# Kernel tuning notes

Measured on AMD Instinct MI355X. Metric: run time of the kernel, lower is better.

Reference implementation:

```python
import jax, jax.numpy as jnp
import numpy as np

D_MODEL = 1024
NUM_HEADS = 16
HEAD_DIM = D_MODEL // NUM_HEADS
CLAMP = 1e9


def setup_inputs() -> dict:
    key = jax.random.key(0)
    ks = jax.random.split(key, 5)
    B, S = 2, 2048
    x = jax.random.normal(ks[0], (B, S, D_MODEL), dtype=jnp.float32)
    # causal mask, broadcastable over [B, H, S, S]
    mask = jnp.tril(jnp.ones((S, S), dtype=bool))
    Wqkv = jax.random.normal(ks[1], (D_MODEL, 3 * D_MODEL), dtype=jnp.float32) * (1.0 / np.sqrt(D_MODEL))
    bqkv = jax.random.normal(ks[2], (3 * D_MODEL,), dtype=jnp.float32) * 0.02
    Wo = jax.random.normal(ks[3], (D_MODEL, D_MODEL), dtype=jnp.float32) * (1.0 / np.sqrt(D_MODEL))
    bo = jax.random.normal(ks[4], (D_MODEL,), dtype=jnp.float32) * 0.02
    return {"x": x, "mask": mask, "Wqkv": Wqkv, "bqkv": bqkv, "Wo": Wo, "bo": bo}


def reference(x, mask, Wqkv, bqkv, Wo, bo):
    B, S, _ = x.shape
    qkv = x @ Wqkv + bqkv                               # [B, S, 3*d_model]
    qkv = qkv.reshape(B, S, NUM_HEADS, 3 * HEAD_DIM).transpose(0, 2, 1, 3)  # [B, H, S, 3*hd]
    q, k, v = jnp.split(qkv, 3, axis=-1)                # each [B, H, S, hd]
    scale = 1.0 / np.sqrt(HEAD_DIM)
    scores = jnp.einsum('bhqd,bhkd->bhqk', q, k) * scale  # [B, H, S, S]
    scores = jnp.where(mask, scores, -jnp.inf)
    scores = jnp.clip(scores, -CLAMP, CLAMP)
    attn = jax.nn.softmax(scores, axis=-1)
    values = jnp.einsum('bhqk,bhkd->bhqd', attn, v)     # [B, H, S, hd]
    values = values.transpose(0, 2, 1, 3).reshape(B, S, D_MODEL)
    return values @ Wo + bo
```

## Files before the change

kernel.cpp:

```cpp
#include <hip/hip_runtime.h>
#include <hip/hip_bf16.h>

#define S_LEN 2048
#define NHEAD 16
#define HDIM  64
#define DMODEL 1024

typedef unsigned short u16;
typedef __attribute__((ext_vector_type(8))) short short8;
typedef __attribute__((ext_vector_type(4))) float floatx4;
typedef __attribute__((ext_vector_type(4))) u16 u16x4;

__device__ __forceinline__ u16 f2bf(float f) {
  unsigned u = __builtin_bit_cast(unsigned, f);
  u += 0x7fffu + ((u >> 16) & 1u);
  return (u16)(u >> 16);
}
__device__ __forceinline__ float bf2f(u16 b) {
  unsigned u = ((unsigned)b) << 16;
  return __builtin_bit_cast(float, u);
}
__device__ __forceinline__ void gload_lds16(const void* g, void* l) {
  __builtin_amdgcn_global_load_lds((const __attribute__((address_space(1))) unsigned int*)g,
                                   (__attribute__((address_space(3))) unsigned int*)l,
                                   16, 0, 0);
}
__device__ __forceinline__ int swz(int b) { return b ^ (((b >> 7) & 7) << 4); }

#define MFMA16(a, b, c) __builtin_amdgcn_mfma_f32_16x16x32_bf16(a, b, c, 0, 0, 0)

__global__ __launch_bounds__(256) void k_prep(const float* __restrict__ x,
                                              const float* __restrict__ Wqkv,
                                              const float* __restrict__ Wo,
                                              u16* __restrict__ xh,
                                              u16* __restrict__ wh,
                                              u16* __restrict__ woh) {
  int bid = blockIdx.x, tid = threadIdx.x;
  if (bid < 4096) {
    int i = (bid * 256 + tid) * 4;
    float4 v = *(const float4*)(x + i);
    u16x4 hv = {f2bf(v.x), f2bf(v.y), f2bf(v.z), f2bf(v.w)};
    *(u16x4*)(xh + i) = hv;
    return;
  }
  __shared__ float t[32][33];
  const float* in; u16* oh; int C, bx, by;
  if (bid < 7168) { int b = bid - 4096; in = Wqkv; oh = wh;  C = 3072; bx = b % 96; by = b / 96; }
  else            { int b = bid - 7168; in = Wo;   oh = woh; C = 1024; bx = b & 31; by = b >> 5; }
  const int R = 1024;
  int c0 = bx * 32, r0 = by * 32;
  int tx = tid & 31, ty = tid >> 5;
#pragma unroll
  for (int rr = ty; rr < 32; rr += 8) t[rr][tx] = in[(size_t)(r0 + rr) * C + c0 + tx];
  __syncthreads();
#pragma unroll
  for (int rr = ty; rr < 32; rr += 8)
    oh[(size_t)(c0 + rr) * R + r0 + tx] = f2bf(t[tx][rr]);
}

__device__ __forceinline__ void gemm_main(const u16* __restrict__ A, const u16* __restrict__ B,
                                          int m0, int n0, floatx4 (&acc)[4][4],
                                          u16* sA, u16* sB) {
  const int tid = threadIdx.x, lane = tid & 63;
  const int wid = tid >> 6, wr = wid >> 1, wc = wid & 1;
  const int cl = lane & 15, hi = lane >> 4;
  const int rmask = ((cl >> 1) & 7) << 4;
  const int aoff = (wr * 4096 + cl * 64 + hi * 16) ^ rmask;
  const int boff = (wc * 4096 + cl * 64 + hi * 16) ^ rmask;
#pragma unroll
  for (int i = 0; i < 4; ++i)
#pragma unroll
    for (int j = 0; j < 4; ++j) acc[i][j] = (floatx4){0.f, 0.f, 0.f, 0.f};

  auto stage = [&](int buf, int kt) {
    int k0 = kt * 32;
#pragma unroll
    for (int it = 0; it < 2; ++it) {
      int p = (it * 256 + tid) * 16;
      int q = swz(p);
      int row = q >> 6, colb = q & 63;
      int base = buf * 8192 + (it * 256 + (tid & ~63)) * 16;
      gload_lds16((const char*)A + (size_t)(m0 + row) * 2048 + k0 * 2 + colb, (char*)sA + base);
      gload_lds16((const char*)B + (size_t)(n0 + row) * 2048 + k0 * 2 + colb, (char*)sB + base);
    }
  };
  stage(0, 0);
  __syncthreads();
  for (int kt = 0; kt < 32; ++kt) {
    int cur = kt & 1;
    if (kt + 1 < 32) stage(cur ^ 1, kt + 1);
    short8 a[4], b[4];
#pragma unroll
    for (int i = 0; i < 4; ++i) {
      a[i] = *(const short8*)((const char*)sA + cur * 8192 + aoff + i * 1024);
      b[i] = *(const short8*)((const char*)sB + cur * 8192 + boff + i * 1024);
    }
    __builtin_amdgcn_s_setprio(1);
#pragma unroll
    for (int i = 0; i < 4; ++i)
#pragma unroll
      for (int j = 0; j < 4; ++j)
        acc[i][j] = MFMA16(a[i], b[j], acc[i][j]);
    __builtin_amdgcn_s_setprio(0);
    __syncthreads();
  }
}

__device__ __forceinline__ void gemm_main_n64(const u16* __restrict__ A, const u16* __restrict__ B,
                                              int m0, int n0, floatx4 (&acc)[4][2]) {
  __shared__ __align__(16) u16 sA[2][128 * 32];
  __shared__ __align__(16) u16 sB[2][64 * 32];
  const int tid = threadIdx.x, lane = tid & 63;
  const int wid = tid >> 6, wr = wid >> 1, wc = wid & 1;
  const int cl = lane & 15, hi = lane >> 4;
  const int rmask = ((cl >> 1) & 7) << 4;
  const int aoff = (wr * 4096 + cl * 64 + hi * 16) ^ rmask;
  const int boff = (wc * 2048 + cl * 64 + hi * 16) ^ rmask;
#pragma unroll
  for (int i = 0; i < 4; ++i)
#pragma unroll
    for (int j = 0; j < 2; ++j) acc[i][j] = (floatx4){0.f, 0.f, 0.f, 0.f};

  auto stage = [&](int buf, int kt) {
    int k0 = kt * 32;
#pragma unroll
    for (int it = 0; it < 2; ++it) {
      int p = (it * 256 + tid) * 16;
      int q = swz(p);
      int row = q >> 6, colb = q & 63;
      int base = (it * 256 + (tid & ~63)) * 16;
      gload_lds16((const char*)A + (size_t)(m0 + row) * 2048 + k0 * 2 + colb, (char*)sA[buf] + base);
    }
    {
      int p = tid * 16;
      int q = swz(p);
      int row = q >> 6, colb = q & 63;
      int base = (tid & ~63) * 16;
      gload_lds16((const char*)B + (size_t)(n0 + row) * 2048 + k0 * 2 + colb, (char*)sB[buf] + base);
    }
  };
  stage(0, 0);
  __syncthreads();
  for (int kt = 0; kt < 32; ++kt) {
    int cur = kt & 1;
    if (kt + 1 < 32) stage(cur ^ 1, kt + 1);
    short8 a[4], b[2];
#pragma unroll
    for (int i = 0; i < 4; ++i)
      a[i] = *(const short8*)((const char*)sA[cur] + aoff + i * 1024);
#pragma unroll
    for (int j = 0; j < 2; ++j)
      b[j] = *(const short8*)((const char*)sB[cur] + boff + j * 1024);
    __builtin_amdgcn_s_setprio(1);
#pragma unroll
    for (int i = 0; i < 4; ++i)
#pragma unroll
      for (int j = 0; j < 2; ++j)
        acc[i][j] = MFMA16(a[i], b[j], acc[i][j]);
    __builtin_amdgcn_s_setprio(0);
    __syncthreads();
  }
}

__global__ __launch_bounds__(256) void k_qkv_gemm(const u16* __restrict__ xh,
                                                  const u16* __restrict__ wh,
                                                  const float* __restrict__ bqkv,
                                                  u16* __restrict__ Qb, u16* __restrict__ Kb,
                                                  u16* __restrict__ Vt) {
  int bid = blockIdx.y * 24 + blockIdx.x;
  int sid = (bid & 7) * 96 + (bid >> 3);
  int m0 = (sid / 24) * 128, n0 = (sid % 24) * 128;
  __shared__ __align__(16) u16 pool[18432];
  floatx4 acc[4][4];
  gemm_main(xh, wh, m0, n0, acc, pool, pool + 8192);
  const int tid = threadIdx.x, lane = tid & 63, wid = tid >> 6;
  const int wr = wid >> 1, wc = wid & 1;
  const int cl = lane & 15, hi = lane >> 4;
  const int nbase = n0 + wc * 64;
  const int h = nbase / 192;
  const int rr0 = nbase - h * 192;
  const int mb = m0 + wr * 64;
  const int b = mb >> 11, s0 = mb & 2047;
  const int bh = b * 16 + h;
  u16* buf = pool + wid * 4608;
  float bias[4];
#pragma unroll
  for (int j = 0; j < 4; ++j) bias[j] = bqkv[nbase + j * 16 + cl];
  if (rr0 < 128) {
#pragma unroll
    for (int j = 0; j < 4; ++j)
#pragma unroll
      for (int i = 0; i < 4; ++i)
#pragma unroll
        for (int r = 0; r < 4; ++r)
          buf[(i * 16 + hi * 4 + r) * 72 + j * 16 + cl] = f2bf(acc[i][j][r] + bias[j]);
    asm volatile("s_waitcnt lgkmcnt(0)" ::: "memory");
    u16* dst0 = (rr0 ? Kb : Qb) + ((size_t)bh * 2048 + s0) * 64;
#pragma unroll
    for (int k = 0; k < 8; ++k) {
      int m_l = k * 8 + (lane >> 3);
      short8 v = *(const short8*)&buf[m_l * 72 + (lane & 7) * 8];
      *(short8*)(dst0 + (size_t)m_l * 64 + (lane & 7) * 8) = v;
    }
  } else {
#pragma unroll
    for (int j = 0; j < 4; ++j)
#pragma unroll
      for (int i = 0; i < 4; ++i)
#pragma unroll
        for (int r = 0; r < 4; ++r)
          buf[(j * 16 + cl) * 72 + i * 16 + hi * 4 + r] = f2bf(acc[i][j][r] + bias[j]);
    asm volatile("s_waitcnt lgkmcnt(0)" ::: "memory");
    u16* dst0 = Vt + (size_t)bh * 64 * 2048 + s0;
#pragma unroll
    for (int k = 0; k < 8; ++k) {
      int nl = k * 8 + (lane >> 3);
      short8 v = *(const short8*)&buf[nl * 72 + (lane & 7) * 8];
      *(short8*)(dst0 + (size_t)nl * 2048 + (lane & 7) * 8) = v;
    }
  }
}

__global__ __launch_bounds__(512, 6) void k_attn(const u16* __restrict__ Qb,
                                                 const u16* __restrict__ Kb,
                                                 const u16* __restrict__ Vt,
                                                 u16* __restrict__ ao,
                                                 u16* __restrict__ pO,
                                                 float* __restrict__ pL) {
  const int bid = blockIdx.x;
  const int bh = (bid & 7) + 8 * ((bid >> 3) / 40);
  const int idx = (bid >> 3) % 40;
  int qt, c;
  if (idx < 4)        { qt = idx;                   c = 0; }
  else if (idx < 12)  { qt = 4 + ((idx - 4) >> 1);  c = (idx - 4) & 1; }
  else if (idx < 24)  { qt = 8 + (idx - 12) / 3;    c = (idx - 12) % 3; }
  else                { qt = 12 + ((idx - 24) >> 2); c = (idx - 24) & 3; }
  const int q0 = qt * 128;
  const int tid = threadIdx.x, lane = tid & 63, wid = tid >> 6;
  const int cl = lane & 15, hi = lane >> 4;
  const int wq0 = q0 + wid * 16;
  const int myq = wq0 + cl;
  const u16* Qp = Qb + (size_t)bh * (S_LEN * HDIM);
  const u16* Kp = Kb + (size_t)bh * (S_LEN * HDIM);
  const u16* Vp = Vt + (size_t)bh * (HDIM * S_LEN);

  __shared__ __align__(16) u16 Kl[2][64 * 64];
  __shared__ __align__(16) u16 Vl[2][64 * 64];
  __shared__ __align__(16) u16 Pl[8][16 * 72];

  const int kvo0 = (cl * 128 + hi * 16) ^ ((cl & 7) << 4);
  const int kvo1 = kvo0 ^ 64;

  short8 qf[2];
#pragma unroll
  for (int kf = 0; kf < 2; ++kf)
    qf[kf] = *(const short8*)&Qp[(size_t)myq * 64 + kf * 32 + hi * 8];

  floatx4 o[4];
#pragma unroll
  for (int fc = 0; fc < 4; ++fc) o[fc] = (floatx4){0.f, 0.f, 0.f, 0.f};
  float lrun = 0.f;

  const int t0 = c * 8;
  const int NTb = min(t0 + 8, 2 * qt + 2);
  const int NTw = 2 * qt + 1 + (wid >> 2);
  const float C1 = 0.125f * 1.44269504f;
  const float C2 = 16.0f * 1.44269504f;

  auto stage = [&](int buf, int kv0) {
    int p = tid * 16;
    int q = swz(p);
    int row = q >> 7, colb = q & 127;
    int base = (tid & ~63) * 16;
    gload_lds16((const char*)Kp + (size_t)(kv0 + row) * 128 + colb, (char*)Kl[buf] + base);
    gload_lds16((const char*)Vp + (size_t)row * 4096 + (size_t)kv0 * 2 + colb, (char*)Vl[buf] + base);
  };
  stage(0, t0 * 64);

  for (int t = t0; t < NTb; ++t) {
    int cur = t & 1;
    asm volatile("s_waitcnt vmcnt(0)" ::: "memory");
    __builtin_amdgcn_s_barrier();
    if (t + 1 < NTb) stage(cur ^ 1, (t + 1) * 64);
    if (t < NTw) {
      int kv0 = t * 64;
      floatx4 sc[4];
#pragma unroll
      for (int fc = 0; fc < 4; ++fc) sc[fc] = (floatx4){0.f, 0.f, 0.f, 0.f};
      __builtin_amdgcn_s_setprio(1);
#pragma unroll
      for (int kf = 0; kf < 2; ++kf) {
        const char* kb = (const char*)Kl[cur] + (kf ? kvo1 : kvo0);
        short8 kfv[4];
#pragma unroll
        for (int fc = 0; fc < 4; ++fc)
          kfv[fc] = *(const short8*)(kb + fc * 2048);
#pragma unroll
        for (int fc = 0; fc < 4; ++fc)
          sc[fc] = MFMA16(kfv[fc], qf[kf], sc[fc]);
      }
      __builtin_amdgcn_s_setprio(0);
      auto smax = [&](bool masked) {
        float ls = 0.f;
#pragma unroll
        for (int fc = 0; fc < 4; ++fc) {
          float p0 = exp2f(sc[fc][0] * C1 - C2);
          float p1 = exp2f(sc[fc][1] * C1 - C2);
          float p2 = exp2f(sc[fc][2] * C1 - C2);
          float p3 = exp2f(sc[fc][3] * C1 - C2);
          if (masked) {
            int key = kv0 + fc * 16 + hi * 4;
            p0 = (key + 0 <= myq) ? p0 : 0.f;
            p1 = (key + 1 <= myq) ? p1 : 0.f;
            p2 = (key + 2 <= myq) ? p2 : 0.f;
            p3 = (key + 3 <= myq) ? p3 : 0.f;
          }
          unsigned r0, r1;
          asm("v_cvt_pk_bf16_f32 %0, %1, %2" : "=v"(r0) : "v"(p0), "v"(p1));
          asm("v_cvt_pk_bf16_f32 %0, %1, %2" : "=v"(r1) : "v"(p2), "v"(p3));
          uint2 rr; rr.x = r0; rr.y = r1;
          *(uint2*)((char*)Pl[wid] + cl * 144 + fc * 32 + hi * 8) = rr;
          ls += (p0 + p1) + (p2 + p3);
        }
        lrun += ls;
      };
      if (t == NTw - 1) smax(true); else smax(false);
      __builtin_amdgcn_s_setprio(1);
#pragma unroll
      for (int kf = 0; kf < 2; ++kf) {
        short8 pa = *(const short8*)((const char*)Pl[wid] + cl * 144 + kf * 64 + hi * 16);
        const char* vbp = (const char*)Vl[cur] + (kf ? kvo1 : kvo0);
        short8 vb[4];
#pragma unroll
        for (int fc = 0; fc < 4; ++fc)
          vb[fc] = *(const short8*)(vbp + fc * 2048);
#pragma unroll
        for (int fc = 0; fc < 4; ++fc)
          o[fc] = MFMA16(pa, vb[fc], o[fc]);
      }
      __builtin_amdgcn_s_setprio(0);
    }
  }
  float l = lrun;
  l += __shfl_xor(l, 16);
  l += __shfl_xor(l, 32);
  if (qt < 4) {
    const int b = bh >> 4, h = bh & 15;
#pragma unroll
    for (int j = 0; j < 4; ++j) {
      float inv = 1.f / __shfl(l, hi * 4 + j);
      int q = wq0 + hi * 4 + j;
#pragma unroll
      for (int fc = 0; fc < 4; ++fc) {
        size_t idx2 = ((size_t)b * 2048 + q) * 1024 + h * 64 + fc * 16 + cl;
        ao[idx2] = f2bf(o[fc][j] * inv);
      }
    }
  } else {
    const int slot = (bh * 12 + (qt - 4)) * 4 + c;
    u16* po = pO + (size_t)slot * 8192 + (size_t)wid * 16 * 64;
    if (hi == 0) pL[slot * 128 + wid * 16 + cl] = l;
#pragma unroll
    for (int j = 0; j < 4; ++j) {
      int row = hi * 4 + j;
#pragma unroll
      for (int fc = 0; fc < 4; ++fc)
        po[row * 64 + fc * 16 + cl] = f2bf(o[fc][j]);
    }
  }
}

__global__ __launch_bounds__(256) void k_attn_reduce(const u16* __restrict__ pO,
                                                     const float* __restrict__ pL,
                                                     u16* __restrict__ ao) {
  int e = blockIdx.x * 256 + threadIdx.x;
  int d0 = (e & 15) * 4;
  int row = (e >> 4) & 127;
  int t = e >> 11;
  int qt = 4 + t % 12;
  int bh = t / 12;
  int nch = (2 * qt + 9) >> 3;
  int slot = t * 4;
  size_t obase = (size_t)slot * 8192 + row * 64 + d0;
  float O0 = 0.f, O1 = 0.f, O2 = 0.f, O3 = 0.f, l = 0.f;
  for (int c = 0; c < nch; ++c) {
    u16x4 v = *(const u16x4*)(pO + obase + (size_t)c * 8192);
    O0 += bf2f(v.x); O1 += bf2f(v.y); O2 += bf2f(v.z); O3 += bf2f(v.w);
    l += pL[(slot + c) * 128 + row];
  }
  float inv = 1.f / l;
  u16x4 r = {f2bf(O0 * inv), f2bf(O1 * inv), f2bf(O2 * inv), f2bf(O3 * inv)};
  int b = bh >> 4, h = bh & 15;
  int q = qt * 128 + row;
  *(u16x4*)(ao + ((size_t)b * 2048 + q) * 1024 + h * 64 + d0) = r;
}

__global__ __launch_bounds__(256) void k_out_gemm(const u16* __restrict__ ao,
                                                  const u16* __restrict__ woh,
                                                  const float* __restrict__ bo, float* __restrict__ out) {
  int bid = blockIdx.x;
  int sid = (bid & 7) * 64 + (bid >> 3);
  int m0 = (sid >> 4) * 128, n0 = (sid & 15) * 64;
  floatx4 acc[4][2];
  gemm_main_n64(ao, woh, m0, n0, acc);
  const int lane = threadIdx.x & 63, wid = threadIdx.x >> 6;
  const int wr = wid >> 1, wc = wid & 1;
#pragma unroll
  for (int j = 0; j < 2; ++j) {
    int n = n0 + wc * 32 + j * 16 + (lane & 15);
    float bias = bo[n];
#pragma unroll
    for (int i = 0; i < 4; ++i) {
#pragma unroll
      for (int r = 0; r < 4; ++r) {
        int m = m0 + wr * 64 + i * 16 + (lane >> 4) * 4 + r;
        out[(size_t)m * 1024 + n] = acc[i][j][r] + bias;
      }
    }
  }
}

extern "C" void kernel_launch(void* const* d_in, const int* in_sizes, int n_in,
                              void* d_out, int out_size, void* d_ws, size_t ws_size,
                              hipStream_t stream) {
  (void)in_sizes; (void)n_in; (void)out_size; (void)ws_size;
  const float* x    = (const float*)d_in[0];
  const float* Wqkv = (const float*)d_in[2];
  const float* bqkv = (const float*)d_in[3];
  const float* Wo   = (const float*)d_in[4];
  const float* bo   = (const float*)d_in[5];
  float* out = (float*)d_out;

  u16* p = (u16*)d_ws;
  u16* xh  = p; p += 4194304;
  u16* wh  = p; p += 3145728;
  u16* woh = p; p += 1048576;
  u16* Qb  = p; p += 4194304;
  u16* Kb  = p; p += 4194304;
  u16* Vt  = p; p += 4194304;
  u16* pO  = p; p += 12582912;
  float* pL = (float*)p; p += 393216;
  u16* ao  = xh;

  k_prep<<<8192, 256, 0, stream>>>(x, Wqkv, Wo, xh, wh, woh);
  k_qkv_gemm<<<dim3(24, 32), 256, 0, stream>>>(xh, wh, bqkv, Qb, Kb, Vt);
  k_attn<<<1280, 512, 0, stream>>>(Qb, Kb, Vt, ao, pO, pL);
  k_attn_reduce<<<3072, 256, 0, stream>>>(pO, pL, ao);
  k_out_gemm<<<512, 256, 0, stream>>>(ao, woh, bo, out);
}
```

Baseline: 117.2 us.

## Double query tile per attention block to reuse K/V tiles across 32 rows per wave

Each attention block now covers 256 query rows with each wave processing two 16-row groups, so every K/V tile staged in LDS feeds twice as many MFMAs. Grid shrinks to 640 blocks with a new split-KV chunk mapping scheduled in reverse (heaviest tiles first), and the partial-output reduce kernel and workspace layout are updated to match. The cost is more registers per thread (occupancy hint lowered from 6 to 4 waves) and fewer blocks to spread across CUs.

```diff
diff --git a/kernel.cpp b/kernel.cpp
--- a/kernel.cpp
+++ b/kernel.cpp
@@ -221,49 +221,56 @@
   }
 }
 
-__global__ __launch_bounds__(512, 6) void k_attn(const u16* __restrict__ Qb,
+__global__ __launch_bounds__(512, 4) void k_attn(const u16* __restrict__ Qb,
                                                  const u16* __restrict__ Kb,
                                                  const u16* __restrict__ Vt,
                                                  u16* __restrict__ ao,
                                                  u16* __restrict__ pO,
                                                  float* __restrict__ pL) {
   const int bid = blockIdx.x;
-  const int bh = (bid & 7) + 8 * ((bid >> 3) / 40);
-  const int idx = (bid >> 3) % 40;
-  int qt, c;
-  if (idx < 4)        { qt = idx;                   c = 0; }
-  else if (idx < 12)  { qt = 4 + ((idx - 4) >> 1);  c = (idx - 4) & 1; }
-  else if (idx < 24)  { qt = 8 + (idx - 12) / 3;    c = (idx - 12) % 3; }
-  else                { qt = 12 + ((idx - 24) >> 2); c = (idx - 24) & 3; }
-  const int q0 = qt * 128;
+  const int bh = (bid & 7) + 8 * ((bid >> 3) / 20);
+  const int ridx = 19 - ((bid >> 3) % 20);
+  int qt2, c;
+  if (ridx < 1)       { qt2 = 0; c = 0; }
+  else if (ridx < 2)  { qt2 = 1; c = 0; }
+  else if (ridx < 4)  { qt2 = 2; c = ridx - 2; }
+  else if (ridx < 6)  { qt2 = 3; c = ridx - 4; }
+  else if (ridx < 9)  { qt2 = 4; c = ridx - 6; }
+  else if (ridx < 12) { qt2 = 5; c = ridx - 9; }
+  else if (ridx < 16) { qt2 = 6; c = ridx - 12; }
+  else                { qt2 = 7; c = ridx - 16; }
+  const int q0 = qt2 * 256;
   const int tid = threadIdx.x, lane = tid & 63, wid = tid >> 6;
   const int cl = lane & 15, hi = lane >> 4;
-  const int wq0 = q0 + wid * 16;
-  const int myq = wq0 + cl;
+  const int wq0 = q0 + wid * 32;
   const u16* Qp = Qb + (size_t)bh * (S_LEN * HDIM);
   const u16* Kp = Kb + (size_t)bh * (S_LEN * HDIM);
   const u16* Vp = Vt + (size_t)bh * (HDIM * S_LEN);
 
   __shared__ __align__(16) u16 Kl[2][64 * 64];
   __shared__ __align__(16) u16 Vl[2][64 * 64];
-  __shared__ __align__(16) u16 Pl[8][16 * 72];
+  __shared__ __align__(16) u16 Pl[8][32 * 72];
 
   const int kvo0 = (cl * 128 + hi * 16) ^ ((cl & 7) << 4);
   const int kvo1 = kvo0 ^ 64;
 
-  short8 qf[2];
-#pragma unroll
-  for (int kf = 0; kf < 2; ++kf)
-    qf[kf] = *(const short8*)&Qp[(size_t)myq * 64 + kf * 32 + hi * 8];
-
-  floatx4 o[4];
-#pragma unroll
-  for (int fc = 0; fc < 4; ++fc) o[fc] = (floatx4){0.f, 0.f, 0.f, 0.f};
-  float lrun = 0.f;
+  short8 qf[2][2];
+#pragma unroll
+  for (int g = 0; g < 2; ++g)
+#pragma unroll
+    for (int kf = 0; kf < 2; ++kf)
+      qf[g][kf] = *(const short8*)&Qp[(size_t)(wq0 + g * 16 + cl) * 64 + kf * 32 + hi * 8];
+
+  floatx4 o[2][4];
+#pragma unroll
+  for (int g = 0; g < 2; ++g)
+#pragma unroll
+    for (int fc = 0; fc < 4; ++fc) o[g][fc] = (floatx4){0.f, 0.f, 0.f, 0.f};
+  float lrun[2] = {0.f, 0.f};
 
   const int t0 = c * 8;
-  const int NTb = min(t0 + 8, 2 * qt + 2);
-  const int NTw = 2 * qt + 1 + (wid >> 2);
+  const int NTb = min(t0 + 8, 4 * qt2 + 4);
+  const int NTw = 4 * qt2 + (wid >> 1) + 1;
   const float C1 = 0.125f * 1.44269504f;
   const float C2 = 16.0f * 1.44269504f;
 
@@ -284,9 +291,11 @@
     if (t + 1 < NTb) stage(cur ^ 1, (t + 1) * 64);
     if (t < NTw) {
       int kv0 = t * 64;
-      floatx4 sc[4];
-#pragma unroll
-      for (int fc = 0; fc < 4; ++fc) sc[fc] = (floatx4){0.f, 0.f, 0.f, 0.f};
+      floatx4 sc[2][4];
+#pragma unroll
+      for (int g = 0; g < 2; ++g)
+#pragma unroll
+        for (int fc = 0; fc < 4; ++fc) sc[g][fc] = (floatx4){0.f, 0.f, 0.f, 0.f};
       __builtin_amdgcn_s_setprio(1);
 #pragma unroll
       for (int kf = 0; kf < 2; ++kf) {
@@ -296,76 +305,91 @@
         for (int fc = 0; fc < 4; ++fc)
           kfv[fc] = *(const short8*)(kb + fc * 2048);
 #pragma unroll
-        for (int fc = 0; fc < 4; ++fc)
-          sc[fc] = MFMA16(kfv[fc], qf[kf], sc[fc]);
+        for (int g = 0; g < 2; ++g)
+#pragma unroll
+          for (int fc = 0; fc < 4; ++fc)
+            sc[g][fc] = MFMA16(kfv[fc], qf[g][kf], sc[g][fc]);
       }
       __builtin_amdgcn_s_setprio(0);
       auto smax = [&](bool masked) {
-        float ls = 0.f;
-#pragma unroll
-        for (int fc = 0; fc < 4; ++fc) {
-          float p0 = exp2f(sc[fc][0] * C1 - C2);
-          float p1 = exp2f(sc[fc][1] * C1 - C2);
-          float p2 = exp2f(sc[fc][2] * C1 - C2);
-          float p3 = exp2f(sc[fc][3] * C1 - C2);
-          if (masked) {
-            int key = kv0 + fc * 16 + hi * 4;
-            p0 = (key + 0 <= myq) ? p0 : 0.f;
-            p1 = (key + 1 <= myq) ? p1 : 0.f;
-            p2 = (key + 2 <= myq) ? p2 : 0.f;
-            p3 = (key + 3 <= myq) ? p3 : 0.f;
+#pragma unroll
+        for (int g = 0; g < 2; ++g) {
+          int myq = wq0 + g * 16 + cl;
+          float ls = 0.f;
+#pragma unroll
+          for (int fc = 0; fc < 4; ++fc) {
+            float p0 = exp2f(sc[g][fc][0] * C1 - C2);
+            float p1 = exp2f(sc[g][fc][1] * C1 - C2);
+            float p2 = exp2f(sc[g][fc][2] * C1 - C2);
+            float p3 = exp2f(sc[g][fc][3] * C1 - C2);
+            if (masked) {
+              int key = kv0 + fc * 16 + hi * 4;
+              p0 = (key + 0 <= myq) ? p0 : 0.f;
+              p1 = (key + 1 <= myq) ? p1 : 0.f;
+              p2 = (key + 2 <= myq) ? p2 : 0.f;
+              p3 = (key + 3 <= myq) ? p3 : 0.f;
+            }
+            unsigned r0, r1;
+            asm("v_cvt_pk_bf16_f32 %0, %1, %2" : "=v"(r0) : "v"(p0), "v"(p1));
+            asm("v_cvt_pk_bf16_f32 %0, %1, %2" : "=v"(r1) : "v"(p2), "v"(p3));
+            uint2 rr; rr.x = r0; rr.y = r1;
+            *(uint2*)((char*)Pl[wid] + (g * 16 + cl) * 144 + fc * 32 + hi * 8) = rr;
+            ls += (p0 + p1) + (p2 + p3);
           }
-          unsigned r0, r1;
-          asm("v_cvt_pk_bf16_f32 %0, %1, %2" : "=v"(r0) : "v"(p0), "v"(p1));
-          asm("v_cvt_pk_bf16_f32 %0, %1, %2" : "=v"(r1) : "v"(p2), "v"(p3));
-          uint2 rr; rr.x = r0; rr.y = r1;
-          *(uint2*)((char*)Pl[wid] + cl * 144 + fc * 32 + hi * 8) = rr;
-          ls += (p0 + p1) + (p2 + p3);
+          lrun[g] += ls;
         }
-        lrun += ls;
       };
       if (t == NTw - 1) smax(true); else smax(false);
       __builtin_amdgcn_s_setprio(1);
 #pragma unroll
       for (int kf = 0; kf < 2; ++kf) {
-        short8 pa = *(const short8*)((const char*)Pl[wid] + cl * 144 + kf * 64 + hi * 16);
         const char* vbp = (const char*)Vl[cur] + (kf ? kvo1 : kvo0);
-        short8 vb[4];
+        short8 pa[2], vb[4];
+#pragma unroll
+        for (int g = 0; g < 2; ++g)
+          pa[g] = *(const short8*)((const char*)Pl[wid] + (g * 16 + cl) * 144 + kf * 64 + hi * 16);
 #pragma unroll
         for (int fc = 0; fc < 4; ++fc)
           vb[fc] = *(const short8*)(vbp + fc * 2048);
 #pragma unroll
-        for (int fc = 0; fc < 4; ++fc)
-          o[fc] = MFMA16(pa, vb[fc], o[fc]);
+        for (int g = 0; g < 2; ++g)
+#pragma unroll
+          for (int fc = 0; fc < 4; ++fc)
+            o[g][fc] = MFMA16(pa[g], vb[fc], o[g][fc]);
       }
       __builtin_amdgcn_s_setprio(0);
     }
   }
-  float l = lrun;
-  l += __shfl_xor(l, 16);
-  l += __shfl_xor(l, 32);
-  if (qt < 4) {
-    const int b = bh >> 4, h = bh & 15;
-#pragma unroll
-    for (int j = 0; j < 4; ++j) {
-      float inv = 1.f / __shfl(l, hi * 4 + j);
-      int q = wq0 + hi * 4 + j;
-#pragma unroll
-      for (int fc = 0; fc < 4; ++fc) {
-        size_t idx2 = ((size_t)b * 2048 + q) * 1024 + h * 64 + fc * 16 + cl;
-        ao[idx2] = f2bf(o[fc][j] * inv);
+  int pbase = (qt2 == 2) ? 0 : (qt2 == 3) ? 2 : (qt2 == 4) ? 4 :
+              (qt2 == 5) ? 7 : (qt2 == 6) ? 10 : 14;
+  const int slot = bh * 18 + pbase + c;
+#pragma unroll
+  for (int g = 0; g < 2; ++g) {
+    float l = lrun[g];
+    l += __shfl_xor(l, 16);
+    l += __shfl_xor(l, 32);
+    if (qt2 < 2) {
+      const int b = bh >> 4, h = bh & 15;
+#pragma unroll
+      for (int j = 0; j < 4; ++j) {
+        float inv = 1.f / __shfl(l, hi * 4 + j);
+        int q = wq0 + g * 16 + hi * 4 + j;
+#pragma unroll
+        for (int fc = 0; fc < 4; ++fc) {
+          size_t idx2 = ((size_t)b * 2048 + q) * 1024 + h * 64 + fc * 16 + cl;
+          ao[idx2] = f2bf(o[g][fc][j] * inv);
+        }
       }
-    }
-  } else {
-    const int slot = (bh * 12 + (qt - 4)) * 4 + c;
-    u16* po = pO + (size_t)slot * 8192 + (size_t)wid * 16 * 64;
-    if (hi == 0) pL[slot * 128 + wid * 16 + cl] = l;
-#pragma unroll
-    for (int j = 0; j < 4; ++j) {
-      int row = hi * 4 + j;
-#pragma unroll
-      for (int fc = 0; fc < 4; ++fc)
-        po[row * 64 + fc * 16 + cl] = f2bf(o[fc][j]);
+    } else {
+      u16* po = pO + (size_t)slot * 16384 + (size_t)(wid * 32 + g * 16) * 64;
+      if (hi == 0) pL[slot * 256 + wid * 32 + g * 16 + cl] = l;
+#pragma unroll
+      for (int j = 0; j < 4; ++j) {
+        int row = hi * 4 + j;
+#pragma unroll
+        for (int fc = 0; fc < 4; ++fc)
+          po[row * 64 + fc * 16 + cl] = f2bf(o[g][fc][j]);
+      }
     }
   }
 }
@@ -375,23 +399,25 @@
                                                      u16* __restrict__ ao) {
   int e = blockIdx.x * 256 + threadIdx.x;
   int d0 = (e & 15) * 4;
-  int row = (e >> 4) & 127;
-  int t = e >> 11;
-  int qt = 4 + t % 12;
-  int bh = t / 12;
-  int nch = (2 * qt + 9) >> 3;
-  int slot = t * 4;
-  size_t obase = (size_t)slot * 8192 + row * 64 + d0;
+  int row = (e >> 4) & 255;
+  int t = e >> 12;
+  int qt2 = 2 + t % 6;
+  int bh = t / 6;
+  int nch = (qt2 >> 1) + 1;
+  int pbase = (qt2 == 2) ? 0 : (qt2 == 3) ? 2 : (qt2 == 4) ? 4 :
+              (qt2 == 5) ? 7 : (qt2 == 6) ? 10 : 14;
+  int slot0 = bh * 18 + pbase;
+  size_t obase = (size_t)slot0 * 16384 + row * 64 + d0;
   float O0 = 0.f, O1 = 0.f, O2 = 0.f, O3 = 0.f, l = 0.f;
   for (int c = 0; c < nch; ++c) {
-    u16x4 v = *(const u16x4*)(pO + obase + (size_t)c * 8192);
+    u16x4 v = *(const u16x4*)(pO + obase + (size_t)c * 16384);
     O0 += bf2f(v.x); O1 += bf2f(v.y); O2 += bf2f(v.z); O3 += bf2f(v.w);
-    l += pL[(slot + c) * 128 + row];
+    l += pL[(slot0 + c) * 256 + row];
   }
   float inv = 1.f / l;
   u16x4 r = {f2bf(O0 * inv), f2bf(O1 * inv), f2bf(O2 * inv), f2bf(O3 * inv)};
   int b = bh >> 4, h = bh & 15;
-  int q = qt * 128 + row;
+  int q = qt2 * 256 + row;
   *(u16x4*)(ao + ((size_t)b * 2048 + q) * 1024 + h * 64 + d0) = r;
 }
 
@@ -438,13 +464,13 @@
   u16* Qb  = p; p += 4194304;
   u16* Kb  = p; p += 4194304;
   u16* Vt  = p; p += 4194304;
-  u16* pO  = p; p += 12582912;
-  float* pL = (float*)p; p += 393216;
+  u16* pO  = p; p += 9437184;
+  float* pL = (float*)p; p += 294912;
   u16* ao  = xh;
 
   k_prep<<<8192, 256, 0, stream>>>(x, Wqkv, Wo, xh, wh, woh);
   k_qkv_gemm<<<dim3(24, 32), 256, 0, stream>>>(xh, wh, bqkv, Qb, Kb, Vt);
-  k_attn<<<1280, 512, 0, stream>>>(Qb, Kb, Vt, ao, pO, pL);
+  k_attn<<<640, 512, 0, stream>>>(Qb, Kb, Vt, ao, pO, pL);
   k_attn_reduce<<<3072, 256, 0, stream>>>(pO, pL, ao);
   k_out_gemm<<<512, 256, 0, stream>>>(ao, woh, bo, out);
 }
```

New measurement: 119.8 us. 1.02x slower.

## Single-buffer V, prefetch K two tiles ahead, swizzle P, reverse block order

Applied to the files above, without the earlier changes.

Restructures the attention KV pipeline. K stays double-buffered and is now prefetched two tiles ahead, while V is single-buffered and reloaded after a second barrier. Partial vmcnt waits let the next K load remain in flight across iterations. P scratch drops its row padding in favour of an XOR swizzle, which together with single-buffered V cuts LDS use so the launch bound can ask for 8 blocks. Block order is reversed so the long causal tiles start first. The cost is an extra barrier per iteration and V loads that are exposed rather than overlapped.

```diff
diff --git a/kernel.cpp b/kernel.cpp
--- a/kernel.cpp
+++ b/kernel.cpp
@@ -221,7 +221,7 @@
   }
 }
 
-__global__ __launch_bounds__(512, 6) void k_attn(const u16* __restrict__ Qb,
+__global__ __launch_bounds__(512, 8) void k_attn(const u16* __restrict__ Qb,
                                                  const u16* __restrict__ Kb,
                                                  const u16* __restrict__ Vt,
                                                  u16* __restrict__ ao,
@@ -229,7 +229,7 @@
                                                  float* __restrict__ pL) {
   const int bid = blockIdx.x;
   const int bh = (bid & 7) + 8 * ((bid >> 3) / 40);
-  const int idx = (bid >> 3) % 40;
+  const int idx = 39 - ((bid >> 3) % 40);
   int qt, c;
   if (idx < 4)        { qt = idx;                   c = 0; }
   else if (idx < 12)  { qt = 4 + ((idx - 4) >> 1);  c = (idx - 4) & 1; }
@@ -245,11 +245,14 @@
   const u16* Vp = Vt + (size_t)bh * (HDIM * S_LEN);
 
   __shared__ __align__(16) u16 Kl[2][64 * 64];
-  __shared__ __align__(16) u16 Vl[2][64 * 64];
-  __shared__ __align__(16) u16 Pl[8][16 * 72];
+  __shared__ __align__(16) u16 Vl[64 * 64];
+  __shared__ __align__(16) u16 Pl[8][16 * 64];
 
   const int kvo0 = (cl * 128 + hi * 16) ^ ((cl & 7) << 4);
   const int kvo1 = kvo0 ^ 64;
+  const int pmask = (cl & 7) << 4;
+  const int pbw = wid * 2048 + cl * 128 + hi * 8;
+  const int pbr = wid * 2048 + cl * 128 + hi * 16;
 
   short8 qf[2];
 #pragma unroll
@@ -267,21 +270,29 @@
   const float C1 = 0.125f * 1.44269504f;
   const float C2 = 16.0f * 1.44269504f;
 
-  auto stage = [&](int buf, int kv0) {
+  auto stageK = [&](int buf, int kv0) {
     int p = tid * 16;
     int q = swz(p);
     int row = q >> 7, colb = q & 127;
     int base = (tid & ~63) * 16;
     gload_lds16((const char*)Kp + (size_t)(kv0 + row) * 128 + colb, (char*)Kl[buf] + base);
-    gload_lds16((const char*)Vp + (size_t)row * 4096 + (size_t)kv0 * 2 + colb, (char*)Vl[buf] + base);
   };
-  stage(0, t0 * 64);
+  auto stageV = [&](int kv0) {
+    int p = tid * 16;
+    int q = swz(p);
+    int row = q >> 7, colb = q & 127;
+    int base = (tid & ~63) * 16;
+    gload_lds16((const char*)Vp + (size_t)row * 4096 + (size_t)kv0 * 2 + colb, (char*)Vl + base);
+  };
+  stageK(0, t0 * 64);
+  stageV(t0 * 64);
+  if (t0 + 1 < NTb) stageK(1, (t0 + 1) * 64);
 
   for (int t = t0; t < NTb; ++t) {
-    int cur = t & 1;
-    asm volatile("s_waitcnt vmcnt(0)" ::: "memory");
+    int cur = (t - t0) & 1;
+    if (t + 1 < NTb) asm volatile("s_waitcnt vmcnt(1)" ::: "memory");
+    else             asm volatile("s_waitcnt vmcnt(0)" ::: "memory");
     __builtin_amdgcn_s_barrier();
-    if (t + 1 < NTb) stage(cur ^ 1, (t + 1) * 64);
     if (t < NTw) {
       int kv0 = t * 64;
       floatx4 sc[4];
@@ -319,7 +330,7 @@
           asm("v_cvt_pk_bf16_f32 %0, %1, %2" : "=v"(r0) : "v"(p0), "v"(p1));
           asm("v_cvt_pk_bf16_f32 %0, %1, %2" : "=v"(r1) : "v"(p2), "v"(p3));
           uint2 rr; rr.x = r0; rr.y = r1;
-          *(uint2*)((char*)Pl[wid] + cl * 144 + fc * 32 + hi * 8) = rr;
+          *(uint2*)((char*)Pl + ((pbw + fc * 32) ^ pmask)) = rr;
           ls += (p0 + p1) + (p2 + p3);
         }
         lrun += ls;
@@ -328,8 +339,8 @@
       __builtin_amdgcn_s_setprio(1);
 #pragma unroll
       for (int kf = 0; kf < 2; ++kf) {
-        short8 pa = *(const short8*)((const char*)Pl[wid] + cl * 144 + kf * 64 + hi * 16);
-        const char* vbp = (const char*)Vl[cur] + (kf ? kvo1 : kvo0);
+        short8 pa = *(const short8*)((const char*)Pl + ((pbr + kf * 64) ^ pmask));
+        const char* vbp = (const char*)Vl + (kf ? kvo1 : kvo0);
         short8 vb[4];
 #pragma unroll
         for (int fc = 0; fc < 4; ++fc)
@@ -340,6 +351,9 @@
       }
       __builtin_amdgcn_s_setprio(0);
     }
+    __builtin_amdgcn_s_barrier();
+    if (t + 1 < NTb) stageV((t + 1) * 64);
+    if (t + 2 < NTb) stageK(cur, (t + 2) * 64);
   }
   float l = lrun;
   l += __shfl_xor(l, 16);
```

Measured after the change: 151.6 us. 1.29x slower.
